# Optimization experiments

Measured on AMD Instinct MI355X. Metric: run time of the kernel, lower is better.

## Reference

```python
import jax, jax.numpy as jnp
import numpy as np

B, S, HID, NH = 4, 4096, 1024, 16
D = HID // NH
EPS = 1e-5


def setup_inputs() -> dict:
    key = jax.random.key(0)
    ks = jax.random.split(key, 8)
    x = jax.random.normal(ks[0], (B, S, HID), dtype=jnp.float32)
    sc = 0.03  # ~xavier for 1024x1024
    Wq = jax.random.normal(ks[1], (HID, HID), dtype=jnp.float32) * sc
    Wk = jax.random.normal(ks[2], (HID, HID), dtype=jnp.float32) * sc
    Wv = jax.random.normal(ks[3], (HID, HID), dtype=jnp.float32) * sc
    Wbeta = jax.random.normal(ks[4], (HID, NH), dtype=jnp.float32) * sc
    b_beta = jnp.full((NH,), 0.9, dtype=jnp.float32)  # init.constant_(0.9)
    Wo = jax.random.normal(ks[5], (HID, HID), dtype=jnp.float32) * sc
    b_o = jnp.zeros((HID,), dtype=jnp.float32)
    ln_g = jnp.ones((HID,), dtype=jnp.float32)
    ln_b = jnp.zeros((HID,), dtype=jnp.float32)
    return {"x": x, "Wq": Wq, "Wk": Wk, "Wv": Wv, "Wbeta": Wbeta,
            "b_beta": b_beta, "Wo": Wo, "b_o": b_o, "ln_g": ln_g, "ln_b": ln_b}


def _delta_scan(q, k, v, beta):
    # q,k,v: (B,S,NH,D); beta: (B,S,NH)
    # Faithful to torch einsum 'bik,bji->bjk' with broadcast over i:
    # update[b,h,:,k'] = k_t[b,h,k'] * sum_d v_t[b,h,d]  (same row repeated)
    vsum = v.sum(-1)  # (B,S,NH)
    qs = jnp.moveaxis(q, 1, 0)       # (S,B,NH,D)
    ks_ = jnp.moveaxis(k, 1, 0)
    vs = jnp.moveaxis(vsum, 1, 0)    # (S,B,NH)
    bs = jnp.moveaxis(beta, 1, 0)    # (S,B,NH)

    def step(h, inp):
        q_t, k_t, vsum_t, beta_t = inp
        h = h * beta_t[..., None, None]
        h = h + (k_t * vsum_t[..., None])[:, :, None, :]  # broadcast over rows
        o_t = jnp.einsum('bhj,bhjk->bhk', q_t, h)
        return h, o_t

    h0 = jnp.zeros((q.shape[0], q.shape[2], D, D), dtype=q.dtype)
    _, o = jax.lax.scan(step, h0, (qs, ks_, vs, bs))
    return jnp.moveaxis(o, 0, 1)  # (B,S,NH,D)


def reference(x, Wq, Wk, Wv, Wbeta, b_beta, Wo, b_o, ln_g, ln_b):
    b, s, hid = x.shape
    residual = x
    q = (x @ Wq).reshape(b, s, NH, D)
    k = (x @ Wk).reshape(b, s, NH, D)
    v = (x @ Wv).reshape(b, s, NH, D)
    beta = jax.nn.sigmoid(x @ Wbeta + b_beta)  # (B,S,NH)
    o = _delta_scan(q, k, v, beta).reshape(b, s, hid)
    out = o @ Wo + b_o  # dropout is identity in eval
    y = residual + out
    mu = y.mean(-1, keepdims=True)
    var = ((y - mu) ** 2).mean(-1, keepdims=True)
    return ln_g * (y - mu) * jax.lax.rsqrt(var + EPS) + ln_b
```

## Files before the change

kernel.cpp:

```cpp
#include <hip/hip_runtime.h>
#include <hip/hip_bf16.h>

typedef unsigned short u16;
typedef unsigned int   u32;
typedef u32 __attribute__((address_space(1))) gas_u32;
typedef u32 __attribute__((address_space(3))) las_u32;
typedef __bf16 bf16x8 __attribute__((ext_vector_type(8)));
typedef float  f32x4  __attribute__((ext_vector_type(4)));

constexpr int BATCH = 4, SEQ = 4096, HID = 1024, NH = 16, DH = 64;
constexpr int M  = BATCH * SEQ;
constexpr int KD = HID;

__device__ __forceinline__ u16 f2bf(float f) {
  __hip_bfloat16 h = __float2bfloat16(f);
  u16 u; __builtin_memcpy(&u, &h, 2); return u;
}
__device__ __forceinline__ float bf2f(u16 u) {
  u32 x = ((u32)u) << 16; float f; __builtin_memcpy(&f, &x, 4); return f;
}


__global__ __launch_bounds__(256) void cast_x_kernel(const float4* __restrict__ x,
                                                     uint4* __restrict__ xb) {
  int i = blockIdx.x * 256 + threadIdx.x;
  float4 a = x[2 * i], b = x[2 * i + 1];
  uint4 o;
  o.x = (u32)f2bf(a.x) | ((u32)f2bf(a.y) << 16);
  o.y = (u32)f2bf(a.z) | ((u32)f2bf(a.w) << 16);
  o.z = (u32)f2bf(b.x) | ((u32)f2bf(b.y) << 16);
  o.w = (u32)f2bf(b.z) | ((u32)f2bf(b.w) << 16);
  xb[i] = o;
}

__global__ __launch_bounds__(256) void transpose_cast(const float* __restrict__ Wk,
                                                      const float* __restrict__ Wo,
                                                      u16* __restrict__ WkT,
                                                      u16* __restrict__ WoT) {
  __shared__ float tile[32][33];
  const float* src = blockIdx.z ? Wo : Wk;
  u16* dst = blockIdx.z ? WoT : WkT;
  int bx = blockIdx.x * 32, by = blockIdx.y * 32;
  int tx = threadIdx.x & 31, ty = threadIdx.x >> 5;
#pragma unroll
  for (int i = 0; i < 4; i++)
    tile[ty + i * 8][tx] = src[(size_t)(by + ty + i * 8) * HID + bx + tx];
  __syncthreads();
#pragma unroll
  for (int i = 0; i < 4; i++)
    dst[(size_t)(bx + ty + i * 8) * HID + by + tx] = f2bf(tile[tx][ty + i * 8]);
}

__global__ __launch_bounds__(256) void build_wsum(const float* __restrict__ Wq,
                                                  const float* __restrict__ Wv,
                                                  const float* __restrict__ Wbeta,
                                                  u16* __restrict__ WsT) {
  int tid = blockIdx.x * 256 + threadIdx.x;
  int c = tid >> 10, kk = tid & 1023;
  float s = 0.f;
  if (c < 16)      { for (int d = 0; d < DH; d++) s += Wq[(size_t)kk * HID + c * DH + d]; }
  else if (c < 32) { for (int d = 0; d < DH; d++) s += Wv[(size_t)kk * HID + (c - 16) * DH + d]; }
  else if (c < 48) { s = Wbeta[(size_t)kk * NH + (c - 32)]; }
  WsT[(size_t)c * HID + kk] = f2bf(s);
}


__device__ __forceinline__ void stage_quarter(const u16* __restrict__ Gk,
                                              int q, u16* lds_tile, int tid, int wave) {
  const int row = q * 64 + (tid >> 3);
  const int s = tid & 7;
  const u16* g = Gk + (size_t)row * KD + (size_t)((s ^ (row & 7)) << 3);
  u16* l = lds_tile + q * 4096 + wave * 512;
  __builtin_amdgcn_global_load_lds((const gas_u32*)g, (las_u32*)l, 16, 0, 0);
}

__device__ __forceinline__ const bf16x8* lds_frag(const u16* lds_tile, int row, int cg) {
  return (const bf16x8*)(lds_tile + ((size_t)row << 6) + (size_t)((cg ^ (row & 7)) << 3));
}

template <int EPI>
__global__ __launch_bounds__(512) void gemm256(
    const u16* __restrict__ A, const u16* __restrict__ Bt, int N,
    u16* __restrict__ Cb, const u16* __restrict__ xres, const float* __restrict__ bias) {
  constexpr int BK = 64, NT = KD / BK;
  __shared__ u16 lds[2][2][16384];
  const int tid = threadIdx.x, wave = tid >> 6, lane = tid & 63;
  const int wm = wave >> 2, wn = wave & 3;
  const int r16 = lane & 15, hi = lane >> 4;
  const int nbn = N >> 8;
  const int bm = (int)blockIdx.x / nbn, bn = (int)blockIdx.x % nbn;
  const u16* Abase = A + (size_t)bm * 256 * KD;
  const u16* Bbase = Bt + (size_t)bn * 256 * KD;

  f32x4 acc[8][4] = {};

  {
    u16* la = &lds[0][0][0]; u16* lb = &lds[0][1][0];
    stage_quarter(Abase, 0, la, tid, wave);
    stage_quarter(Abase, 2, la, tid, wave);
    stage_quarter(Bbase, 0, lb, tid, wave);
    stage_quarter(Bbase, 1, lb, tid, wave);
    stage_quarter(Bbase, 2, lb, tid, wave);
    stage_quarter(Bbase, 3, lb, tid, wave);
    stage_quarter(Abase, 1, la, tid, wave);
    stage_quarter(Abase, 3, la, tid, wave);
  }
  asm volatile("s_waitcnt vmcnt(2)" ::: "memory");
  __builtin_amdgcn_s_barrier();

  for (int kt = 0; kt < NT; ++kt) {
    const int cur = kt & 1;
    const u16* la = &lds[cur][0][0];
    const u16* lb = &lds[cur][1][0];
    u16* na = &lds[cur ^ 1][0][0];
    u16* nb = &lds[cur ^ 1][1][0];
    const int knext = ((kt + 1) & (NT - 1)) * BK;
    const u16* An = Abase + knext;
    const u16* Bn = Bbase + knext;

    bf16x8 bF[4][2];
#pragma unroll
    for (int ph = 0; ph < 4; ++ph) {
      const int mh = ph >> 1;
      const int kk = ph & 1;
      if (ph == 0)      { stage_quarter(An, 0, na, tid, wave); stage_quarter(An, 2, na, tid, wave); }
      else if (ph == 1) { stage_quarter(Bn, 0, nb, tid, wave); stage_quarter(Bn, 1, nb, tid, wave); }
      else if (ph == 2) { stage_quarter(Bn, 2, nb, tid, wave); stage_quarter(Bn, 3, nb, tid, wave); }
      else              { stage_quarter(An, 1, na, tid, wave); stage_quarter(An, 3, na, tid, wave); }
      bf16x8 aF[4];
#pragma unroll
      for (int f = 0; f < 4; ++f)
        aF[f] = *lds_frag(la, wm * 128 + mh * 64 + f * 16 + r16, kk * 4 + hi);
      if (ph < 2) {
#pragma unroll
        for (int g = 0; g < 4; ++g)
          bF[g][kk] = *lds_frag(lb, wn * 64 + g * 16 + r16, kk * 4 + hi);
      }
      __builtin_amdgcn_s_barrier();
      asm volatile("s_waitcnt lgkmcnt(0)" ::: "memory");
      __builtin_amdgcn_sched_barrier(0);
      __builtin_amdgcn_s_setprio(1);
#pragma unroll
      for (int f = 0; f < 4; ++f)
#pragma unroll
        for (int g = 0; g < 4; ++g)
          acc[mh * 4 + f][g] = __builtin_amdgcn_mfma_f32_16x16x32_bf16(
              aF[f], bF[g][kk], acc[mh * 4 + f][g], 0, 0, 0);
      __builtin_amdgcn_s_setprio(0);
      if (ph == 1) { asm volatile("s_waitcnt vmcnt(4)" ::: "memory"); }
      if (ph == 3) { asm volatile("s_waitcnt vmcnt(2)" ::: "memory"); }
      __builtin_amdgcn_s_barrier();
    }
  }
  asm volatile("s_waitcnt vmcnt(0)" ::: "memory");

#pragma unroll
  for (int fm = 0; fm < 8; ++fm) {
#pragma unroll
    for (int fn = 0; fn < 4; ++fn) {
      const int col = bn * 256 + wn * 64 + fn * 16 + r16;
#pragma unroll
      for (int j = 0; j < 4; ++j) {
        const int row = bm * 256 + wm * 128 + fm * 16 + hi * 4 + j;
        float v = acc[fm][fn][j];
        if constexpr (EPI == 2) v += bf2f(xres[(size_t)row * N + col]) + bias[col];
        Cb[(size_t)row * N + col] = f2bf(v);
      }
    }
  }
}

__global__ __launch_bounds__(256) void gemm_skinny(
    const u16* __restrict__ A, const u16* __restrict__ Bt,
    const float* __restrict__ bias, float* __restrict__ sq,
    float* __restrict__ sv, float* __restrict__ sb) {
  constexpr int BM = 128, BN = 64, BK = 64;
  constexpr int WTM = 32, FM = 2, FN = 4;
  __shared__ u16 As[BM * BK];
  __shared__ u16 Bs[BN * BK];
  const int tid = threadIdx.x, wave = tid >> 6, lane = tid & 63;
  const int bm = blockIdx.x;
  const int r16 = lane & 15, hi = lane >> 4;
  const int rsub = lane >> 3, csub = (lane & 7) * 8;
  f32x4 acc[FM][FN] = {};
  const u16* Ab = A + (size_t)bm * BM * KD;

  for (int kt = 0; kt < KD; kt += BK) {
#pragma unroll
    for (int i = 0; i < 4; i++) {
      int slot = wave * 4 + i;
      const u16* g = Ab + (size_t)(slot * 8 + rsub) * KD + kt + csub;
      __builtin_amdgcn_global_load_lds((const gas_u32*)g, (las_u32*)(As + slot * 512), 16, 0, 0);
    }
#pragma unroll
    for (int i = 0; i < 2; i++) {
      int slot = wave * 2 + i;
      const u16* g = Bt + (size_t)(slot * 8 + rsub) * KD + kt + csub;
      __builtin_amdgcn_global_load_lds((const gas_u32*)g, (las_u32*)(Bs + slot * 512), 16, 0, 0);
    }
    __syncthreads();
#pragma unroll
    for (int kk = 0; kk < 2; kk++) {
      bf16x8 af[FM], bfr[FN];
#pragma unroll
      for (int f = 0; f < FM; f++)
        af[f] = *(const bf16x8*)(As + (wave * WTM + f * 16 + r16) * BK + kk * 32 + hi * 8);
#pragma unroll
      for (int f = 0; f < FN; f++)
        bfr[f] = *(const bf16x8*)(Bs + (f * 16 + r16) * BK + kk * 32 + hi * 8);
#pragma unroll
      for (int fm = 0; fm < FM; fm++)
#pragma unroll
        for (int fn = 0; fn < FN; fn++)
          acc[fm][fn] = __builtin_amdgcn_mfma_f32_16x16x32_bf16(af[fm], bfr[fn], acc[fm][fn], 0, 0, 0);
    }
    __syncthreads();
  }

#pragma unroll
  for (int fm = 0; fm < FM; fm++) {
#pragma unroll
    for (int fn = 0; fn < FN; fn++) {
      const int col = fn * 16 + r16;
#pragma unroll
      for (int j = 0; j < 4; j++) {
        const int row = bm * BM + wave * WTM + fm * 16 + hi * 4 + j;
        const int b = row >> 12, t = row & 4095;
        float v = acc[fm][fn][j];
        if (col < 16)      sq[((size_t)(b * 16 + col)) * SEQ + t] = v;
        else if (col < 32) sv[((size_t)(b * 16 + col - 16)) * SEQ + t] = v;
        else if (col < 48) {
          float z = v + bias[col - 32];
          sb[((size_t)(b * 16 + col - 32)) * SEQ + t] = 1.f / (1.f + __expf(-z));
        }
      }
    }
  }
}


__global__ __launch_bounds__(256) void scan_chunks(const u16* __restrict__ kbuf,
                                                   const float* __restrict__ sv_t,
                                                   const float* __restrict__ sb_t,
                                                   float* __restrict__ Pbuf,
                                                   float* __restrict__ Rloc) {
  const int wave = threadIdx.x >> 6, lane = threadIdx.x & 63;
  const int gid = blockIdx.x * 4 + wave;
  const int seq = gid >> 6, chunk = gid & 63;
  const int b = seq >> 4, h = seq & 15;
  const int t0 = chunk * 64;
  const float bet = sb_t[(size_t)seq * SEQ + t0 + lane];
  const float vs  = sv_t[(size_t)seq * SEQ + t0 + lane];
  const u16* kp = kbuf + ((size_t)(b * SEQ + t0)) * HID + h * DH + lane;
  float r = 0.f, P = 1.f;
#pragma unroll
  for (int tt = 0; tt < 64; tt += 8) {
    u16 kr[8];
#pragma unroll
    for (int j = 0; j < 8; j++) kr[j] = kp[(size_t)(tt + j) * HID];
#pragma unroll
    for (int j = 0; j < 8; j++) {
      float bt = __shfl(bet, tt + j);
      float vt = __shfl(vs, tt + j);
      r = fmaf(r, bt, bf2f(kr[j]) * vt);
      P *= bt;
    }
  }
  Rloc[(size_t)gid * 64 + lane] = r;
  if (lane == 0) Pbuf[gid] = P;
}

__global__ __launch_bounds__(64) void scan_prefix(const float* __restrict__ Pbuf,
                                                  const float* __restrict__ Rloc,
                                                  float* __restrict__ Rin) {
  const int seq = blockIdx.x, lane = threadIdx.x;
  const float* pp = Pbuf + seq * 64;
  const float* rl = Rloc + (size_t)seq * 64 * 64 + lane;
  float* ri = Rin + (size_t)seq * 64 * 64 + lane;
  float rin = 0.f;
#pragma unroll
  for (int c0 = 0; c0 < 64; c0 += 8) {
    float P[8], L[8];
#pragma unroll
    for (int j = 0; j < 8; j++) { P[j] = pp[c0 + j]; L[j] = rl[(size_t)(c0 + j) * 64]; }
#pragma unroll
    for (int j = 0; j < 8; j++) {
      ri[(size_t)(c0 + j) * 64] = rin;
      rin = fmaf(P[j], rin, L[j]);
    }
  }
}

__global__ __launch_bounds__(256) void scan_apply(const u16* __restrict__ kbuf,
                                                  const float* __restrict__ sq_t,
                                                  const float* __restrict__ sv_t,
                                                  const float* __restrict__ sb_t,
                                                  const float* __restrict__ Rin,
                                                  u16* __restrict__ obuf) {
  const int wave = threadIdx.x >> 6, lane = threadIdx.x & 63;
  const int gid = blockIdx.x * 4 + wave;
  const int seq = gid >> 6, chunk = gid & 63;
  const int b = seq >> 4, h = seq & 15;
  const int t0 = chunk * 64;
  const float bet = sb_t[(size_t)seq * SEQ + t0 + lane];
  const float vs  = sv_t[(size_t)seq * SEQ + t0 + lane];
  const float qs  = sq_t[(size_t)seq * SEQ + t0 + lane];
  const u16* kp = kbuf + ((size_t)(b * SEQ + t0)) * HID + h * DH + lane;
  u16* op = obuf + ((size_t)(b * SEQ + t0)) * HID + h * DH + lane;
  float r = Rin[(size_t)gid * 64 + lane];
#pragma unroll
  for (int tt = 0; tt < 64; tt += 8) {
    u16 kr[8];
#pragma unroll
    for (int j = 0; j < 8; j++) kr[j] = kp[(size_t)(tt + j) * HID];
#pragma unroll
    for (int j = 0; j < 8; j++) {
      float bt = __shfl(bet, tt + j);
      float vt = __shfl(vs, tt + j);
      float qt = __shfl(qs, tt + j);
      r = fmaf(r, bt, bf2f(kr[j]) * vt);
      op[(size_t)(tt + j) * HID] = f2bf(qt * r);
    }
  }
}

__global__ __launch_bounds__(256) void ln_kernel(const u16* __restrict__ y,
                                                 const float* __restrict__ g,
                                                 const float* __restrict__ bt,
                                                 float* __restrict__ out) {
  const int row = blockIdx.x;
  const u16* yr = y + (size_t)row * HID;
  const int t = threadIdx.x;
  ushort4 u = *(const ushort4*)(yr + t * 4);
  float v0 = bf2f(u.x), v1 = bf2f(u.y), v2 = bf2f(u.z), v3 = bf2f(u.w);
  float s  = v0 + v1 + v2 + v3;
  float ss = v0 * v0 + v1 * v1 + v2 * v2 + v3 * v3;
#pragma unroll
  for (int m = 1; m < 64; m <<= 1) { s += __shfl_xor(s, m); ss += __shfl_xor(ss, m); }
  __shared__ float red[8];
  const int wave = t >> 6, lane = t & 63;
  if (lane == 0) { red[wave] = s; red[4 + wave] = ss; }
  __syncthreads();
  float st  = red[0] + red[1] + red[2] + red[3];
  float sst = red[4] + red[5] + red[6] + red[7];
  float mu  = st * (1.f / 1024.f);
  float var = sst * (1.f / 1024.f) - mu * mu;
  float inv = rsqrtf(var + 1e-5f);
  const int c = t * 4;
  float4 o;
  o.x = g[c + 0] * ((v0 - mu) * inv) + bt[c + 0];
  o.y = g[c + 1] * ((v1 - mu) * inv) + bt[c + 1];
  o.z = g[c + 2] * ((v2 - mu) * inv) + bt[c + 2];
  o.w = g[c + 3] * ((v3 - mu) * inv) + bt[c + 3];
  *(float4*)(out + (size_t)row * HID + c) = o;
}

extern "C" void kernel_launch(void* const* d_in, const int* in_sizes, int n_in,
                              void* d_out, int out_size, void* d_ws, size_t ws_size,
                              hipStream_t stream) {
  const float* x     = (const float*)d_in[0];
  const float* Wq    = (const float*)d_in[1];
  const float* Wk    = (const float*)d_in[2];
  const float* Wv    = (const float*)d_in[3];
  const float* Wbeta = (const float*)d_in[4];
  const float* bbeta = (const float*)d_in[5];
  const float* Wo    = (const float*)d_in[6];
  const float* b_o   = (const float*)d_in[7];
  const float* ln_g  = (const float*)d_in[8];
  const float* ln_b  = (const float*)d_in[9];
  float* out = (float*)d_out;

  char* ws = (char*)d_ws;
  size_t off = 0;
  auto alloc = [&](size_t bytes) {
    char* p = ws + off; off += (bytes + 255) & ~(size_t)255; return p;
  };
  u16* xb   = (u16*)alloc((size_t)M * HID * 2);
  u16* kbuf = (u16*)alloc((size_t)M * HID * 2);
  u16* obuf = (u16*)alloc((size_t)M * HID * 2);
  u16* WkT  = (u16*)alloc((size_t)HID * HID * 2);
  u16* WoT  = (u16*)alloc((size_t)HID * HID * 2);
  u16* WsT  = (u16*)alloc((size_t)64 * HID * 2);
  float* sq_t = (float*)alloc((size_t)64 * SEQ * 4);
  float* sv_t = (float*)alloc((size_t)64 * SEQ * 4);
  float* sb_t = (float*)alloc((size_t)64 * SEQ * 4);
  float* Pbuf = (float*)alloc((size_t)4096 * 4);
  float* Rloc = (float*)alloc((size_t)4096 * 64 * 4);
  float* Rin  = (float*)alloc((size_t)4096 * 64 * 4);
  u16* ybuf = kbuf;

  cast_x_kernel<<<8192, 256, 0, stream>>>((const float4*)x, (uint4*)xb);
  transpose_cast<<<dim3(32, 32, 2), 256, 0, stream>>>(Wk, Wo, WkT, WoT);
  build_wsum<<<256, 256, 0, stream>>>(Wq, Wv, Wbeta, WsT);

  gemm_skinny<<<M / 128, 256, 0, stream>>>(xb, WsT, bbeta, sq_t, sv_t, sb_t);

  gemm256<0><<<(M / 256) * (HID / 256), 512, 0, stream>>>(
      xb, WkT, HID, kbuf, nullptr, nullptr);

  scan_chunks<<<1024, 256, 0, stream>>>(kbuf, sv_t, sb_t, Pbuf, Rloc);
  scan_prefix<<<64, 64, 0, stream>>>(Pbuf, Rloc, Rin);
  scan_apply<<<1024, 256, 0, stream>>>(kbuf, sq_t, sv_t, sb_t, Rin, obuf);

  gemm256<2><<<(M / 256) * (HID / 256), 512, 0, stream>>>(
      obuf, WoT, HID, ybuf, xb, b_o);

  ln_kernel<<<M, 256, 0, stream>>>(ybuf, ln_g, ln_b, out);
}
```

Before: 163.1 us.

## Fuse x bf16 cast into skinny GEMM and peel last GEMM iteration

Removes the standalone cast kernel. The skinny projection GEMM now reads fp32 x directly, converts it to bf16 in registers, stores the tile to LDS and also writes the bf16 copy to global memory for the later K GEMM. The skinny kernel's tile shrinks to 64 rows, giving more blocks. Separately, the large GEMM peels its last K iteration so it no longer issues wasted prefetch loads that wrapped around to tile zero. The cost is that the skinny kernel's A loads are now synchronous register loads instead of async LDS loads.

```diff
diff --git a/kernel.cpp b/kernel.cpp
--- a/kernel.cpp
+++ b/kernel.cpp
@@ -20,18 +20,6 @@
   u32 x = ((u32)u) << 16; float f; __builtin_memcpy(&f, &x, 4); return f;
 }
 
-
-__global__ __launch_bounds__(256) void cast_x_kernel(const float4* __restrict__ x,
-                                                     uint4* __restrict__ xb) {
-  int i = blockIdx.x * 256 + threadIdx.x;
-  float4 a = x[2 * i], b = x[2 * i + 1];
-  uint4 o;
-  o.x = (u32)f2bf(a.x) | ((u32)f2bf(a.y) << 16);
-  o.y = (u32)f2bf(a.z) | ((u32)f2bf(a.w) << 16);
-  o.z = (u32)f2bf(b.x) | ((u32)f2bf(b.y) << 16);
-  o.w = (u32)f2bf(b.z) | ((u32)f2bf(b.w) << 16);
-  xb[i] = o;
-}
 
 __global__ __launch_bounds__(256) void transpose_cast(const float* __restrict__ Wk,
                                                       const float* __restrict__ Wo,
@@ -62,6 +50,73 @@
   else if (c < 32) { for (int d = 0; d < DH; d++) s += Wv[(size_t)kk * HID + (c - 16) * DH + d]; }
   else if (c < 48) { s = Wbeta[(size_t)kk * NH + (c - 32)]; }
   WsT[(size_t)c * HID + kk] = f2bf(s);
+}
+
+__global__ __launch_bounds__(256) void skinny_fused(
+    const float* __restrict__ x, const u16* __restrict__ Bt,
+    const float* __restrict__ bias, float* __restrict__ sq,
+    float* __restrict__ sv, float* __restrict__ sb, u16* __restrict__ xb) {
+  constexpr int BM = 64, BK = 64;
+  __shared__ u16 As[BM * BK];
+  __shared__ u16 Bs[64 * BK];
+  const int tid = threadIdx.x, wave = tid >> 6, lane = tid & 63;
+  const int bm = blockIdx.x;
+  const int r16 = lane & 15, hi = lane >> 4;
+  const int rsub = lane >> 3, csub = (lane & 7) * 8;
+  f32x4 acc[4] = {};
+  const float* Ab = x + (size_t)bm * BM * KD;
+  u16* xbb = xb + (size_t)bm * BM * KD;
+
+  for (int kt = 0; kt < KD; kt += BK) {
+#pragma unroll
+    for (int i = 0; i < 2; i++) {
+      int slot = wave * 2 + i;
+      const u16* g = Bt + (size_t)(slot * 8 + rsub) * KD + kt + csub;
+      __builtin_amdgcn_global_load_lds((const gas_u32*)g, (las_u32*)(Bs + slot * 512), 16, 0, 0);
+    }
+#pragma unroll
+    for (int p = 0; p < 2; p++) {
+      const int row = p * 32 + (tid >> 3);
+      const int c8 = (tid & 7) * 8;
+      const float4 u0 = *(const float4*)(Ab + (size_t)row * KD + kt + c8);
+      const float4 u1 = *(const float4*)(Ab + (size_t)row * KD + kt + c8 + 4);
+      uint4 w;
+      w.x = (u32)f2bf(u0.x) | ((u32)f2bf(u0.y) << 16);
+      w.y = (u32)f2bf(u0.z) | ((u32)f2bf(u0.w) << 16);
+      w.z = (u32)f2bf(u1.x) | ((u32)f2bf(u1.y) << 16);
+      w.w = (u32)f2bf(u1.z) | ((u32)f2bf(u1.w) << 16);
+      *(uint4*)(As + row * BK + c8) = w;
+      *(uint4*)(xbb + (size_t)row * KD + kt + c8) = w;
+    }
+    __syncthreads();
+#pragma unroll
+    for (int kk = 0; kk < 2; kk++) {
+      bf16x8 af = *(const bf16x8*)(As + (wave * 16 + r16) * BK + kk * 32 + hi * 8);
+#pragma unroll
+      for (int fn = 0; fn < 4; fn++) {
+        bf16x8 bfr = *(const bf16x8*)(Bs + (fn * 16 + r16) * BK + kk * 32 + hi * 8);
+        acc[fn] = __builtin_amdgcn_mfma_f32_16x16x32_bf16(af, bfr, acc[fn], 0, 0, 0);
+      }
+    }
+    __syncthreads();
+  }
+
+#pragma unroll
+  for (int fn = 0; fn < 4; fn++) {
+    const int col = fn * 16 + r16;
+#pragma unroll
+    for (int j = 0; j < 4; j++) {
+      const int row = bm * BM + wave * 16 + hi * 4 + j;
+      const int b = row >> 12, t = row & 4095;
+      float v = acc[fn][j];
+      if (col < 16)      sq[((size_t)(b * 16 + col)) * SEQ + t] = v;
+      else if (col < 32) sv[((size_t)(b * 16 + col - 16)) * SEQ + t] = v;
+      else if (col < 48) {
+        float z = v + bias[col - 32];
+        sb[((size_t)(b * 16 + col - 32)) * SEQ + t] = 1.f / (1.f + __expf(-z));
+      }
+    }
+  }
 }
 
 
@@ -108,15 +163,14 @@
   asm volatile("s_waitcnt vmcnt(2)" ::: "memory");
   __builtin_amdgcn_s_barrier();
 
-  for (int kt = 0; kt < NT; ++kt) {
+  for (int kt = 0; kt < NT - 1; ++kt) {
     const int cur = kt & 1;
     const u16* la = &lds[cur][0][0];
     const u16* lb = &lds[cur][1][0];
     u16* na = &lds[cur ^ 1][0][0];
     u16* nb = &lds[cur ^ 1][1][0];
-    const int knext = ((kt + 1) & (NT - 1)) * BK;
-    const u16* An = Abase + knext;
-    const u16* Bn = Bbase + knext;
+    const u16* An = Abase + (kt + 1) * BK;
+    const u16* Bn = Bbase + (kt + 1) * BK;
 
     bf16x8 bF[4][2];
 #pragma unroll
@@ -152,7 +206,38 @@
       __builtin_amdgcn_s_barrier();
     }
   }
-  asm volatile("s_waitcnt vmcnt(0)" ::: "memory");
+
+  {
+    const u16* la = &lds[(NT - 1) & 1][0][0];
+    const u16* lb = &lds[(NT - 1) & 1][1][0];
+    bf16x8 bF[4][2];
+#pragma unroll
+    for (int ph = 0; ph < 4; ++ph) {
+      const int mh = ph >> 1, kk = ph & 1;
+      bf16x8 aF[4];
+#pragma unroll
+      for (int f = 0; f < 4; ++f)
+        aF[f] = *lds_frag(la, wm * 128 + mh * 64 + f * 16 + r16, kk * 4 + hi);
+      if (ph < 2) {
+#pragma unroll
+        for (int g = 0; g < 4; ++g)
+          bF[g][kk] = *lds_frag(lb, wn * 64 + g * 16 + r16, kk * 4 + hi);
+      }
+      __builtin_amdgcn_s_barrier();
+      asm volatile("s_waitcnt lgkmcnt(0)" ::: "memory");
+      __builtin_amdgcn_sched_barrier(0);
+      __builtin_amdgcn_s_setprio(1);
+#pragma unroll
+      for (int f = 0; f < 4; ++f)
+#pragma unroll
+        for (int g = 0; g < 4; ++g)
+          acc[mh * 4 + f][g] = __builtin_amdgcn_mfma_f32_16x16x32_bf16(
+              aF[f], bF[g][kk], acc[mh * 4 + f][g], 0, 0, 0);
+      __builtin_amdgcn_s_setprio(0);
+      if (ph == 1) { asm volatile("s_waitcnt vmcnt(0)" ::: "memory"); }
+      __builtin_amdgcn_s_barrier();
+    }
+  }
 
 #pragma unroll
   for (int fm = 0; fm < 8; ++fm) {
@@ -165,74 +250,6 @@
         float v = acc[fm][fn][j];
         if constexpr (EPI == 2) v += bf2f(xres[(size_t)row * N + col]) + bias[col];
         Cb[(size_t)row * N + col] = f2bf(v);
-      }
-    }
-  }
-}
-
-__global__ __launch_bounds__(256) void gemm_skinny(
-    const u16* __restrict__ A, const u16* __restrict__ Bt,
-    const float* __restrict__ bias, float* __restrict__ sq,
-    float* __restrict__ sv, float* __restrict__ sb) {
-  constexpr int BM = 128, BN = 64, BK = 64;
-  constexpr int WTM = 32, FM = 2, FN = 4;
-  __shared__ u16 As[BM * BK];
-  __shared__ u16 Bs[BN * BK];
-  const int tid = threadIdx.x, wave = tid >> 6, lane = tid & 63;
-  const int bm = blockIdx.x;
-  const int r16 = lane & 15, hi = lane >> 4;
-  const int rsub = lane >> 3, csub = (lane & 7) * 8;
-  f32x4 acc[FM][FN] = {};
-  const u16* Ab = A + (size_t)bm * BM * KD;
-
-  for (int kt = 0; kt < KD; kt += BK) {
-#pragma unroll
-    for (int i = 0; i < 4; i++) {
-      int slot = wave * 4 + i;
-      const u16* g = Ab + (size_t)(slot * 8 + rsub) * KD + kt + csub;
-      __builtin_amdgcn_global_load_lds((const gas_u32*)g, (las_u32*)(As + slot * 512), 16, 0, 0);
-    }
-#pragma unroll
-    for (int i = 0; i < 2; i++) {
-      int slot = wave * 2 + i;
-      const u16* g = Bt + (size_t)(slot * 8 + rsub) * KD + kt + csub;
-      __builtin_amdgcn_global_load_lds((const gas_u32*)g, (las_u32*)(Bs + slot * 512), 16, 0, 0);
-    }
-    __syncthreads();
-#pragma unroll
-    for (int kk = 0; kk < 2; kk++) {
-      bf16x8 af[FM], bfr[FN];
-#pragma unroll
-      for (int f = 0; f < FM; f++)
-        af[f] = *(const bf16x8*)(As + (wave * WTM + f * 16 + r16) * BK + kk * 32 + hi * 8);
-#pragma unroll
-      for (int f = 0; f < FN; f++)
-        bfr[f] = *(const bf16x8*)(Bs + (f * 16 + r16) * BK + kk * 32 + hi * 8);
-#pragma unroll
-      for (int fm = 0; fm < FM; fm++)
-#pragma unroll
-        for (int fn = 0; fn < FN; fn++)
-          acc[fm][fn] = __builtin_amdgcn_mfma_f32_16x16x32_bf16(af[fm], bfr[fn], acc[fm][fn], 0, 0, 0);
-    }
-    __syncthreads();
-  }
-
-#pragma unroll
-  for (int fm = 0; fm < FM; fm++) {
-#pragma unroll
-    for (int fn = 0; fn < FN; fn++) {
-      const int col = fn * 16 + r16;
-#pragma unroll
-      for (int j = 0; j < 4; j++) {
-        const int row = bm * BM + wave * WTM + fm * 16 + hi * 4 + j;
-        const int b = row >> 12, t = row & 4095;
-        float v = acc[fm][fn][j];
-        if (col < 16)      sq[((size_t)(b * 16 + col)) * SEQ + t] = v;
-        else if (col < 32) sv[((size_t)(b * 16 + col - 16)) * SEQ + t] = v;
-        else if (col < 48) {
-          float z = v + bias[col - 32];
-          sb[((size_t)(b * 16 + col - 32)) * SEQ + t] = 1.f / (1.f + __expf(-z));
-        }
       }
     }
   }
@@ -389,11 +406,10 @@
   float* Rin  = (float*)alloc((size_t)4096 * 64 * 4);
   u16* ybuf = kbuf;
 
-  cast_x_kernel<<<8192, 256, 0, stream>>>((const float4*)x, (uint4*)xb);
   transpose_cast<<<dim3(32, 32, 2), 256, 0, stream>>>(Wk, Wo, WkT, WoT);
   build_wsum<<<256, 256, 0, stream>>>(Wq, Wv, Wbeta, WsT);
 
-  gemm_skinny<<<M / 128, 256, 0, stream>>>(xb, WsT, bbeta, sq_t, sv_t, sb_t);
+  skinny_fused<<<M / 64, 256, 0, stream>>>(x, WsT, bbeta, sq_t, sv_t, sb_t, xb);
 
   gemm256<0><<<(M / 256) * (HID / 256), 512, 0, stream>>>(
       xb, WkT, HID, kbuf, nullptr, nullptr);
```

New measurement: 158.4 us. 2.9% less time.
